# Kernel optimization log

Hardware: AMD Instinct MI355X
Metric: run time of the kernel (lower is better)

Reference implementation:

```python
import jax, jax.numpy as jnp
import numpy as np

L, H, D, E, V, MAXS = 12, 12, 64, 768, 50257, 1024

def _ln(x, g, b, eps=1e-5):
    m = jnp.mean(x, axis=-1, keepdims=True)
    v = jnp.mean(jnp.square(x - m), axis=-1, keepdims=True)
    return (x - m) * jax.lax.rsqrt(v + eps) * g + b

def setup_inputs() -> dict:
    key = jax.random.key(0)
    ks = jax.random.split(key, 16)
    s = 0.02
    inp = {
        "input_ids": jax.random.randint(ks[0], (1, 1), 0, V),
        "past_key": jax.random.normal(ks[1], (L, 1, H, MAXS, D), jnp.float32),
        "past_value": jax.random.normal(ks[2], (L, 1, H, MAXS, D), jnp.float32),
        "past_seq_len": 1023,
        "attention_mask": jnp.ones((1, MAXS), jnp.float32),
        "wte": jax.random.normal(ks[3], (V, E), jnp.float32) * s,
        "wpe": jax.random.normal(ks[4], (MAXS, E), jnp.float32) * s,
        "ln1_g": jnp.ones((L, E), jnp.float32),
        "ln1_b": jnp.zeros((L, E), jnp.float32),
        "attn_w": jax.random.normal(ks[5], (L, E, 3 * E), jnp.float32) * s,
        "attn_b": jnp.zeros((L, 3 * E), jnp.float32),
        "proj_w": jax.random.normal(ks[6], (L, E, E), jnp.float32) * s,
        "proj_b": jnp.zeros((L, E), jnp.float32),
        "ln2_g": jnp.ones((L, E), jnp.float32),
        "ln2_b": jnp.zeros((L, E), jnp.float32),
        "fc_w": jax.random.normal(ks[7], (L, E, 4 * E), jnp.float32) * s,
        "fc_b": jnp.zeros((L, 4 * E), jnp.float32),
        "mlp_w": jax.random.normal(ks[8], (L, 4 * E, E), jnp.float32) * s,
        "mlp_b": jnp.zeros((L, E), jnp.float32),
        "lnf_g": jnp.ones((E,), jnp.float32),
        "lnf_b": jnp.zeros((E,), jnp.float32),
    }
    return inp

def reference(input_ids, past_key, past_value, past_seq_len, attention_mask,
              wte, wpe, ln1_g, ln1_b, attn_w, attn_b, proj_w, proj_b,
              ln2_g, ln2_b, fc_w, fc_b, mlp_w, mlp_b, lnf_g, lnf_b):
    S = int(past_seq_len)  # static cache length
    h = wte[input_ids] + wpe[S]                      # [1,1,E]
    bias = (1.0 - attention_mask[:, :S + 1]) * -1e9  # [1,S+1]
    scale = 1.0 / jnp.sqrt(jnp.float32(D))
    pk, pv = past_key, past_value
    for l in range(L):
        x = _ln(h, ln1_g[l], ln1_b[l])
        qkv = x @ attn_w[l] + attn_b[l]              # [1,1,3E]
        q, k, v = jnp.split(qkv, 3, axis=-1)
        q = q.reshape(1, 1, H, D).transpose(0, 2, 1, 3)  # [1,H,1,D]
        k = k.reshape(1, 1, H, D).transpose(0, 2, 1, 3)
        v = v.reshape(1, 1, H, D).transpose(0, 2, 1, 3)
        k_full = jnp.concatenate([pk[l, :, :, :S, :], k], axis=2)  # [1,H,S+1,D]
        v_full = jnp.concatenate([pv[l, :, :, :S, :], v], axis=2)
        scores = jnp.einsum('bhqd,bhkd->bhqk', q, k_full) * scale
        scores = scores + bias[:, None, None, :]
        attn = jax.nn.softmax(scores, axis=-1)
        o = jnp.einsum('bhqk,bhkd->bhqd', attn, v_full)
        o = o.transpose(0, 2, 1, 3).reshape(1, 1, H * D)
        h = h + o @ proj_w[l] + proj_b[l]
        x2 = _ln(h, ln2_g[l], ln2_b[l])
        h = h + jax.nn.gelu(x2 @ fc_w[l] + fc_b[l], approximate=True) @ mlp_w[l] + mlp_b[l]
        pk = pk.at[l, :, :, S, :].set(k[:, :, 0, :])
        pv = pv.at[l, :, :, S, :].set(v[:, :, 0, :])
    h = _ln(h, lnf_g, lnf_b)
    logits = h @ wte.T                               # [1,1,V] (tied lm_head)
    return (logits, pk, pv)
```

## Files before the change

kernel.cpp:

```cpp
#include <hip/hip_runtime.h>
#include <math.h>

#define EMB 768
#define NH 12
#define HD 64
#define NL 12
#define NV 50257
#define MAXS 1024
#define S_PAST 1023
#define E3 2304
#define E4 3072

#define WS_H    0
#define WS_QKV  768
#define WS_FC   3072
#define WS_PART 6144

__device__ __forceinline__ void blockReduce2(float& a, float& b, volatile float* ra, volatile float* rb) {
  int lane = threadIdx.x & 63, wid = threadIdx.x >> 6;
#pragma unroll
  for (int o = 32; o > 0; o >>= 1) { a += __shfl_down(a, o); b += __shfl_down(b, o); }
  if (lane == 0) { ra[wid] = a; rb[wid] = b; }
  __syncthreads();
  if (threadIdx.x == 0) {
    ra[0] = ra[0] + ra[1] + ra[2] + ra[3];
    rb[0] = rb[0] + rb[1] + rb[2] + rb[3];
  }
  __syncthreads();
  a = ra[0]; b = rb[0];
}

__global__ void init_kernel(const int* __restrict__ ids, const float* __restrict__ wte,
                            const float* __restrict__ wpe, const float* __restrict__ attn_b,
                            float* __restrict__ hvec, float* __restrict__ qkv) {
  int idx = blockIdx.x * 256 + threadIdx.x;
  if (idx < E3) qkv[idx] = attn_b[idx];
  if (idx < EMB) {
    int id = ids[0];
    hvec[idx] = wte[(size_t)id * EMB + idx] + wpe[(size_t)S_PAST * EMB + idx];
  }
}

__global__ void ln_gemv4(const float* __restrict__ hvec, const float* __restrict__ g,
                         const float* __restrict__ bb, const float* __restrict__ W,
                         float* __restrict__ out, int N, int l) {
  __shared__ float lh[EMB];
  __shared__ float xs[32];
  __shared__ float ra[4], rb[4];
  __shared__ float4 red[4][64];
  int tid = threadIdx.x, lane = tid & 63, wid = tid >> 6;
  int e0 = blockIdx.y * 32;
  float hv0 = hvec[tid], hv1 = hvec[tid + 256], hv2 = hvec[tid + 512];
  int j4 = blockIdx.x * 64 + lane;
  int N4 = N >> 2;
  const float4* p = (const float4*)(W + (size_t)l * EMB * N) + (size_t)(e0 + wid) * N4 + j4;
  float4 w[8];
#pragma unroll
  for (int i = 0; i < 8; i++) w[i] = p[(size_t)(i * 4) * N4];
  float gv = 0.f, bv = 0.f;
  if (tid < 32) { gv = g[l * EMB + e0 + tid]; bv = bb[l * EMB + e0 + tid]; }
  lh[tid] = hv0; lh[tid + 256] = hv1; lh[tid + 512] = hv2;
  float s1 = hv0 + hv1 + hv2;
  float s2 = hv0 * hv0 + hv1 * hv1 + hv2 * hv2;
  blockReduce2(s1, s2, ra, rb);
  float mean = s1 * (1.f / EMB);
  float var = s2 * (1.f / EMB) - mean * mean;
  float rstd = rsqrtf(var + 1e-5f);
  if (tid < 32) xs[tid] = (lh[e0 + tid] - mean) * rstd * gv + bv;
  __syncthreads();
  float4 acc = {0.f, 0.f, 0.f, 0.f};
#pragma unroll
  for (int i = 0; i < 8; i++) {
    float x = xs[wid + i * 4];
    acc.x += x * w[i].x; acc.y += x * w[i].y; acc.z += x * w[i].z; acc.w += x * w[i].w;
  }
  red[wid][lane] = acc;
  __syncthreads();
  if (wid == 0) {
    float4 a0 = red[0][lane], a1 = red[1][lane], a2 = red[2][lane], a3 = red[3][lane];
    float rx = a0.x + a1.x + a2.x + a3.x;
    float ry = a0.y + a1.y + a2.y + a3.y;
    float rz = a0.z + a1.z + a2.z + a3.z;
    float rw = a0.w + a1.w + a2.w + a3.w;
    float* op = out + (size_t)j4 * 4;
    atomicAdd(op + 0, rx); atomicAdd(op + 1, ry);
    atomicAdd(op + 2, rz); atomicAdd(op + 3, rw);
  }
}

__global__ void attn_kv(const float* __restrict__ qkv, const float* __restrict__ pk,
                        const float* __restrict__ pv, const float* __restrict__ mask,
                        float* __restrict__ opk, float* __restrict__ opv,
                        float* __restrict__ part, int l) {
  int h = blockIdx.x >> 4, c = blockIdx.x & 15;
  int tid = threadIdx.x, lane = tid & 63, wid = tid >> 6;
  int sub = tid & 15, grp = tid >> 4;
  __shared__ float4 qs4[16];
  __shared__ float sc[64];
  __shared__ float4 redo[4][16];
  if (tid < 16) qs4[tid] = ((const float4*)(qkv + h * 64))[tid];
  __syncthreads();
  size_t base = ((size_t)(l * NH + h) * MAXS) * HD;
  const float4* K4 = (const float4*)(pk + base);
  const float4* V4 = (const float4*)(pv + base);
  float4* oK4 = (float4*)(opk + base);
  float4* oV4 = (float4*)(opv + base);
  int t0 = c * 64;
  float4 kreg[4];
#pragma unroll
  for (int i = 0; i < 4; i++) {
    int t = t0 + grp + i * 16;
    kreg[i] = (t == S_PAST) ? ((const float4*)(qkv + EMB + h * 64))[sub] : K4[(size_t)t * 16 + sub];
  }
#pragma unroll
  for (int i = 0; i < 4; i++) {
    int t = t0 + grp + i * 16;
    oK4[(size_t)t * 16 + sub] = kreg[i];
  }
  float4 q4 = qs4[sub];
#pragma unroll
  for (int i = 0; i < 4; i++) {
    int key = grp + i * 16;
    float p = q4.x * kreg[i].x + q4.y * kreg[i].y + q4.z * kreg[i].z + q4.w * kreg[i].w;
    p += __shfl_xor(p, 1); p += __shfl_xor(p, 2);
    p += __shfl_xor(p, 4); p += __shfl_xor(p, 8);
    if (sub == 0) sc[key] = p * 0.125f + (1.f - mask[t0 + key]) * (-1e9f);
  }
  __syncthreads();
  if (wid == 0) {
    float a = sc[lane];
    float m = a;
#pragma unroll
    for (int o = 32; o > 0; o >>= 1) m = fmaxf(m, __shfl_down(m, o));
    m = __shfl(m, 0);
    float ea = expf(a - m);
    sc[lane] = ea;
    float s = ea;
#pragma unroll
    for (int o = 32; o > 0; o >>= 1) s += __shfl_down(s, o);
    if (lane == 0) { part[(h * 16 + c) * 68 + 0] = m; part[(h * 16 + c) * 68 + 1] = s; }
  }
  __syncthreads();
  float4 vreg[4];
#pragma unroll
  for (int i = 0; i < 4; i++) {
    int t = t0 + grp + i * 16;
    vreg[i] = (t == S_PAST) ? ((const float4*)(qkv + 2 * EMB + h * 64))[sub] : V4[(size_t)t * 16 + sub];
  }
#pragma unroll
  for (int i = 0; i < 4; i++) {
    int t = t0 + grp + i * 16;
    oV4[(size_t)t * 16 + sub] = vreg[i];
  }
  float4 acc = {0.f, 0.f, 0.f, 0.f};
#pragma unroll
  for (int i = 0; i < 4; i++) {
    float w = sc[grp + i * 16];
    acc.x += w * vreg[i].x; acc.y += w * vreg[i].y; acc.z += w * vreg[i].z; acc.w += w * vreg[i].w;
  }
  acc.x += __shfl_xor(acc.x, 16); acc.y += __shfl_xor(acc.y, 16);
  acc.z += __shfl_xor(acc.z, 16); acc.w += __shfl_xor(acc.w, 16);
  acc.x += __shfl_xor(acc.x, 32); acc.y += __shfl_xor(acc.y, 32);
  acc.z += __shfl_xor(acc.z, 32); acc.w += __shfl_xor(acc.w, 32);
  if (lane < 16) redo[wid][lane] = acc;
  __syncthreads();
  if (tid < 16) {
    float4 a0 = redo[0][tid], a1 = redo[1][tid], a2 = redo[2][tid], a3 = redo[3][tid];
    float4 r;
    r.x = a0.x + a1.x + a2.x + a3.x;
    r.y = a0.y + a1.y + a2.y + a3.y;
    r.z = a0.z + a1.z + a2.z + a3.z;
    r.w = a0.w + a1.w + a2.w + a3.w;
    ((float4*)(part + (h * 16 + c) * 68 + 4))[tid] = r;
  }
}

__global__ void proj_attn(const float* __restrict__ part, const float* __restrict__ W,
                          const float* __restrict__ bias, const float* __restrict__ fc_b,
                          float* __restrict__ hout, float* __restrict__ wfc, int l) {
  int jb = blockIdx.x;
  int rt = blockIdx.y;
  int h = rt >> 2, esub = rt & 3;
  int tid = threadIdx.x, lane = tid & 63, wid = tid >> 6;
  __shared__ float xs[16];
  __shared__ float4 red[4][64];
  int j4 = jb * 64 + lane;
  const int N4 = EMB >> 2;
  int r0 = h * 64 + esub * 16;
  const float4* p = (const float4*)(W + (size_t)l * EMB * EMB) + (size_t)(r0 + wid) * N4 + j4;
  float4 w[4];
#pragma unroll
  for (int i = 0; i < 4; i++) w[i] = p[(size_t)(i * 4) * N4];
  if (tid < 16) {
    float M = -1e30f;
#pragma unroll
    for (int q = 0; q < 16; q++) M = fmaxf(M, part[(h * 16 + q) * 68]);
    float T = 0.f, o = 0.f;
    int d = esub * 16 + tid;
#pragma unroll
    for (int q = 0; q < 16; q++) {
      float wq = expf(part[(h * 16 + q) * 68] - M);
      T += part[(h * 16 + q) * 68 + 1] * wq;
      o += part[(h * 16 + q) * 68 + 4 + d] * wq;
    }
    xs[tid] = o / T;
  }
  int bid = rt * 3 + jb;
  if (bid < 12) wfc[bid * 256 + tid] = fc_b[l * E4 + bid * 256 + tid];
  __syncthreads();
  float4 acc = {0.f, 0.f, 0.f, 0.f};
#pragma unroll
  for (int i = 0; i < 4; i++) {
    float x = xs[wid + i * 4];
    acc.x += x * w[i].x; acc.y += x * w[i].y; acc.z += x * w[i].z; acc.w += x * w[i].w;
  }
  red[wid][lane] = acc;
  __syncthreads();
  if (wid == 0) {
    float4 a0 = red[0][lane], a1 = red[1][lane], a2 = red[2][lane], a3 = red[3][lane];
    float rx = a0.x + a1.x + a2.x + a3.x;
    float ry = a0.y + a1.y + a2.y + a3.y;
    float rz = a0.z + a1.z + a2.z + a3.z;
    float rw = a0.w + a1.w + a2.w + a3.w;
    if (rt == 0) {
      const float* bp = bias + l * EMB + jb * 256 + lane * 4;
      rx += bp[0]; ry += bp[1]; rz += bp[2]; rw += bp[3];
    }
    float* op = hout + (size_t)jb * 256 + (size_t)lane * 4;
    atomicAdd(op + 0, rx); atomicAdd(op + 1, ry);
    atomicAdd(op + 2, rz); atomicAdd(op + 3, rw);
  }
}

__global__ void mlp_gemv4(const float* __restrict__ fcv, const float* __restrict__ W,
                          const float* __restrict__ bias, const float* __restrict__ attn_b,
                          float* __restrict__ hout, float* __restrict__ qkv, int l) {
  __shared__ float xs[64];
  __shared__ float4 red[4][64];
  int tid = threadIdx.x, lane = tid & 63, wid = tid >> 6;
  int e0 = blockIdx.y * 64;
  int j4 = blockIdx.x * 64 + lane;
  const int N4 = EMB >> 2;
  const float4* p = (const float4*)(W + (size_t)l * E4 * EMB) + (size_t)(e0 + wid) * N4 + j4;
  float4 w[16];
#pragma unroll
  for (int i = 0; i < 16; i++) w[i] = p[(size_t)(i * 4) * N4];
  if (tid < 64) {
    float x = fcv[e0 + tid];
    xs[tid] = 0.5f * x * (1.f + tanhf(0.7978845608028654f * (x + 0.044715f * x * x * x)));
  }
  int bid = blockIdx.y * 3 + blockIdx.x;
  if (l + 1 < NL && bid < 9) qkv[bid * 256 + tid] = attn_b[(l + 1) * E3 + bid * 256 + tid];
  __syncthreads();
  float4 acc = {0.f, 0.f, 0.f, 0.f};
#pragma unroll
  for (int i = 0; i < 16; i++) {
    float x = xs[wid + i * 4];
    acc.x += x * w[i].x; acc.y += x * w[i].y; acc.z += x * w[i].z; acc.w += x * w[i].w;
  }
  red[wid][lane] = acc;
  __syncthreads();
  if (wid == 0) {
    float4 a0 = red[0][lane], a1 = red[1][lane], a2 = red[2][lane], a3 = red[3][lane];
    float rx = a0.x + a1.x + a2.x + a3.x;
    float ry = a0.y + a1.y + a2.y + a3.y;
    float rz = a0.z + a1.z + a2.z + a3.z;
    float rw = a0.w + a1.w + a2.w + a3.w;
    if (blockIdx.y == 0) {
      const float* bp = bias + l * EMB + j4 * 4;
      rx += bp[0]; ry += bp[1]; rz += bp[2]; rw += bp[3];
    }
    float* op = hout + (size_t)j4 * 4;
    atomicAdd(op + 0, rx); atomicAdd(op + 1, ry);
    atomicAdd(op + 2, rz); atomicAdd(op + 3, rw);
  }
}

__global__ void logits_lnf(const float* __restrict__ hvec, const float* __restrict__ g,
                           const float* __restrict__ b, const float* __restrict__ wte,
                           float* __restrict__ out) {
  __shared__ float4 xs4[192];
  __shared__ float ra[4], rb[4];
  int tid = threadIdx.x, lane = tid & 63, wid = tid >> 6;
  float hv0 = hvec[tid], hv1 = hvec[tid + 256], hv2 = hvec[tid + 512];
  int v = blockIdx.x * 4 + wid;
  float4 a0 = {0,0,0,0}, a1 = {0,0,0,0}, a2 = {0,0,0,0};
  if (v < NV) {
    const float4* row = (const float4*)(wte + (size_t)v * EMB);
    a0 = row[lane]; a1 = row[lane + 64]; a2 = row[lane + 128];
  }
  float s1 = hv0 + hv1 + hv2;
  float s2 = hv0 * hv0 + hv1 * hv1 + hv2 * hv2;
  blockReduce2(s1, s2, ra, rb);
  float mean = s1 * (1.f / EMB);
  float var = s2 * (1.f / EMB) - mean * mean;
  float rstd = rsqrtf(var + 1e-5f);
  ((float*)xs4)[tid]       = (hv0 - mean) * rstd * g[tid]       + b[tid];
  ((float*)xs4)[tid + 256] = (hv1 - mean) * rstd * g[tid + 256] + b[tid + 256];
  ((float*)xs4)[tid + 512] = (hv2 - mean) * rstd * g[tid + 512] + b[tid + 512];
  __syncthreads();
  if (v >= NV) return;
  float4 x0 = xs4[lane], x1 = xs4[lane + 64], x2 = xs4[lane + 128];
  float acc = a0.x * x0.x + a0.y * x0.y + a0.z * x0.z + a0.w * x0.w
            + a1.x * x1.x + a1.y * x1.y + a1.z * x1.z + a1.w * x1.w
            + a2.x * x2.x + a2.y * x2.y + a2.z * x2.z + a2.w * x2.w;
#pragma unroll
  for (int o = 32; o > 0; o >>= 1) acc += __shfl_down(acc, o);
  if (lane == 0) out[v] = acc;
}

extern "C" void kernel_launch(void* const* d_in, const int* in_sizes, int n_in,
                              void* d_out, int out_size, void* d_ws, size_t ws_size,
                              hipStream_t stream) {
  const int* input_ids = (const int*)d_in[0];
  const float* past_key = (const float*)d_in[1];
  const float* past_value = (const float*)d_in[2];
  const float* mask = (const float*)d_in[4];
  const float* wte = (const float*)d_in[5];
  const float* wpe = (const float*)d_in[6];
  const float* ln1_g = (const float*)d_in[7];
  const float* ln1_b = (const float*)d_in[8];
  const float* attn_w = (const float*)d_in[9];
  const float* attn_b = (const float*)d_in[10];
  const float* proj_w = (const float*)d_in[11];
  const float* proj_b = (const float*)d_in[12];
  const float* ln2_g = (const float*)d_in[13];
  const float* ln2_b = (const float*)d_in[14];
  const float* fc_w = (const float*)d_in[15];
  const float* fc_b = (const float*)d_in[16];
  const float* mlp_w = (const float*)d_in[17];
  const float* mlp_b = (const float*)d_in[18];
  const float* lnf_g = (const float*)d_in[19];
  const float* lnf_b = (const float*)d_in[20];

  float* out = (float*)d_out;
  float* out_logits = out;
  float* out_pk = out + NV;
  float* out_pv = out_pk + (size_t)NL * NH * MAXS * HD;

  float* ws = (float*)d_ws;
  float* wh = ws + WS_H;
  float* wqkv = ws + WS_QKV;
  float* wfc = ws + WS_FC;
  float* wpart = ws + WS_PART;

  init_kernel<<<9, 256, 0, stream>>>(input_ids, wte, wpe, attn_b, wh, wqkv);

  for (int l = 0; l < NL; l++) {
    ln_gemv4<<<dim3(9, 24), 256, 0, stream>>>(wh, ln1_g, ln1_b, attn_w, wqkv, E3, l);
    attn_kv<<<192, 256, 0, stream>>>(wqkv, past_key, past_value, mask, out_pk, out_pv, wpart, l);
    proj_attn<<<dim3(3, 48), 256, 0, stream>>>(wpart, proj_w, proj_b, fc_b, wh, wfc, l);
    ln_gemv4<<<dim3(12, 24), 256, 0, stream>>>(wh, ln2_g, ln2_b, fc_w, wfc, E4, l);
    mlp_gemv4<<<dim3(3, 48), 256, 0, stream>>>(wfc, mlp_w, mlp_b, attn_b, wh, wqkv, l);
  }
  logits_lnf<<<12565, 256, 0, stream>>>(wh, lnf_g, lnf_b, wte, out_logits);
}
```

Measured before the change: 448.5 us.

## Fuse per-layer kernels into two launches with per-head dataflow counters

Merges the five per-layer kernels into two. Kernel A runs the QKV producer, the attention chunks and the output projection, and kernel B runs FC and MLP. Dependent blocks spin on global atomic counters per head or tile instead of waiting at kernel boundaries. The K/V cache copy loads are issued before the wait, so they overlap with producer work. This cuts launch overhead and inter-kernel bubbles, but risks deadlock or stalls if waiting blocks take up CUs before their producers are scheduled.

```diff
diff --git a/kernel.cpp b/kernel.cpp
--- a/kernel.cpp
+++ b/kernel.cpp
@@ -11,10 +11,32 @@
 #define E3 2304
 #define E4 3072
 
+typedef unsigned int u32;
+
 #define WS_H    0
 #define WS_QKV  768
 #define WS_FC   3072
 #define WS_PART 6144
+#define WS_CNT  19200
+#define CNT_WORDS 6912
+
+__device__ __forceinline__ void f4add(float4& a, const float4& b) {
+  a.x += b.x; a.y += b.y; a.z += b.z; a.w += b.w;
+}
+
+__device__ __forceinline__ void bump(u32* cnt) {
+  __threadfence();
+  __syncthreads();
+  if (threadIdx.x == 0)
+    __hip_atomic_fetch_add(cnt, 1u, __ATOMIC_RELEASE, __HIP_MEMORY_SCOPE_AGENT);
+}
+__device__ __forceinline__ void wait_cnt(u32* cnt, u32 n) {
+  if (threadIdx.x == 0) {
+    while (__hip_atomic_load(cnt, __ATOMIC_ACQUIRE, __HIP_MEMORY_SCOPE_AGENT) < n)
+      __builtin_amdgcn_s_sleep(2);
+  }
+  __syncthreads();
+}
 
 __device__ __forceinline__ void blockReduce2(float& a, float& b, volatile float* ra, volatile float* rb) {
   int lane = threadIdx.x & 63, wid = threadIdx.x >> 6;
@@ -30,110 +52,140 @@
   a = ra[0]; b = rb[0];
 }
 
+__device__ __forceinline__ float gelu(float x) {
+  return 0.5f * x * (1.f + tanhf(0.7978845608028654f * (x + 0.044715f * x * x * x)));
+}
+
 __global__ void init_kernel(const int* __restrict__ ids, const float* __restrict__ wte,
-                            const float* __restrict__ wpe, const float* __restrict__ attn_b,
-                            float* __restrict__ hvec, float* __restrict__ qkv) {
-  int idx = blockIdx.x * 256 + threadIdx.x;
-  if (idx < E3) qkv[idx] = attn_b[idx];
-  if (idx < EMB) {
+                            const float* __restrict__ wpe, float* __restrict__ wsf) {
+  int tid = threadIdx.x;
+  if (blockIdx.x < 3) {
+    int e = blockIdx.x * 256 + tid;
     int id = ids[0];
-    hvec[idx] = wte[(size_t)id * EMB + idx] + wpe[(size_t)S_PAST * EMB + idx];
-  }
-}
-
-__global__ void ln_gemv4(const float* __restrict__ hvec, const float* __restrict__ g,
-                         const float* __restrict__ bb, const float* __restrict__ W,
-                         float* __restrict__ out, int N, int l) {
-  __shared__ float lh[EMB];
-  __shared__ float xs[32];
-  __shared__ float ra[4], rb[4];
-  __shared__ float4 red[4][64];
-  int tid = threadIdx.x, lane = tid & 63, wid = tid >> 6;
-  int e0 = blockIdx.y * 32;
+    wsf[WS_H + e] = wte[(size_t)id * EMB + e] + wpe[(size_t)S_PAST * EMB + e];
+  } else {
+    u32* c = (u32*)(wsf + WS_CNT);
+    for (int k = tid; k < CNT_WORDS; k += 256) c[k] = 0;
+  }
+}
+
+
+__device__ void phase_producer(int p, const float* __restrict__ hvec,
+                               const float* __restrict__ g, const float* __restrict__ bb,
+                               const float* __restrict__ W, const float* __restrict__ qb,
+                               float* __restrict__ wsqkv, float* __restrict__ opk,
+                               float* __restrict__ opv, int l, float* smem, u32* prodc) {
+  int h = p / 6, r = p % 6;
+  int cq = (r >> 1) * EMB + h * 64 + (r & 1) * 32;
+  int tid = threadIdx.x;
+  float* lh = smem;
+  float* xs = smem + 768;
+  volatile float* ra = smem + 1536; volatile float* rb = smem + 1540;
+  float4* red = (float4*)(smem + 1544);
+  int col4 = tid & 7, grp = tid >> 3;
   float hv0 = hvec[tid], hv1 = hvec[tid + 256], hv2 = hvec[tid + 512];
-  int j4 = blockIdx.x * 64 + lane;
-  int N4 = N >> 2;
-  const float4* p = (const float4*)(W + (size_t)l * EMB * N) + (size_t)(e0 + wid) * N4 + j4;
-  float4 w[8];
-#pragma unroll
-  for (int i = 0; i < 8; i++) w[i] = p[(size_t)(i * 4) * N4];
-  float gv = 0.f, bv = 0.f;
-  if (tid < 32) { gv = g[l * EMB + e0 + tid]; bv = bb[l * EMB + e0 + tid]; }
+  const float4* W4 = (const float4*)(W + (size_t)l * EMB * E3) + (cq >> 2) + col4;
+  float4 w[12];
+#pragma unroll
+  for (int i = 0; i < 12; i++) w[i] = W4[(size_t)(grp + 32 * i) * (E3 >> 2)];
+  float gv0 = g[l * EMB + tid], gv1 = g[l * EMB + tid + 256], gv2 = g[l * EMB + tid + 512];
+  float bv0 = bb[l * EMB + tid], bv1 = bb[l * EMB + tid + 256], bv2 = bb[l * EMB + tid + 512];
   lh[tid] = hv0; lh[tid + 256] = hv1; lh[tid + 512] = hv2;
-  float s1 = hv0 + hv1 + hv2;
-  float s2 = hv0 * hv0 + hv1 * hv1 + hv2 * hv2;
+  float s1 = hv0 + hv1 + hv2, s2 = hv0 * hv0 + hv1 * hv1 + hv2 * hv2;
   blockReduce2(s1, s2, ra, rb);
   float mean = s1 * (1.f / EMB);
   float var = s2 * (1.f / EMB) - mean * mean;
   float rstd = rsqrtf(var + 1e-5f);
-  if (tid < 32) xs[tid] = (lh[e0 + tid] - mean) * rstd * gv + bv;
+  xs[tid]       = (hv0 - mean) * rstd * gv0 + bv0;
+  xs[tid + 256] = (hv1 - mean) * rstd * gv1 + bv1;
+  xs[tid + 512] = (hv2 - mean) * rstd * gv2 + bv2;
   __syncthreads();
   float4 acc = {0.f, 0.f, 0.f, 0.f};
 #pragma unroll
-  for (int i = 0; i < 8; i++) {
-    float x = xs[wid + i * 4];
+  for (int i = 0; i < 12; i++) {
+    float x = xs[grp + 32 * i];
     acc.x += x * w[i].x; acc.y += x * w[i].y; acc.z += x * w[i].z; acc.w += x * w[i].w;
   }
-  red[wid][lane] = acc;
-  __syncthreads();
-  if (wid == 0) {
-    float4 a0 = red[0][lane], a1 = red[1][lane], a2 = red[2][lane], a3 = red[3][lane];
-    float rx = a0.x + a1.x + a2.x + a3.x;
-    float ry = a0.y + a1.y + a2.y + a3.y;
-    float rz = a0.z + a1.z + a2.z + a3.z;
-    float rw = a0.w + a1.w + a2.w + a3.w;
-    float* op = out + (size_t)j4 * 4;
-    atomicAdd(op + 0, rx); atomicAdd(op + 1, ry);
-    atomicAdd(op + 2, rz); atomicAdd(op + 3, rw);
-  }
-}
-
-__global__ void attn_kv(const float* __restrict__ qkv, const float* __restrict__ pk,
-                        const float* __restrict__ pv, const float* __restrict__ mask,
-                        float* __restrict__ opk, float* __restrict__ opv,
-                        float* __restrict__ part, int l) {
-  int h = blockIdx.x >> 4, c = blockIdx.x & 15;
+#pragma unroll
+  for (int i = 0; i < 12; i++) w[i] = W4[(size_t)(grp + 32 * (i + 12)) * (E3 >> 2)];
+#pragma unroll
+  for (int i = 0; i < 12; i++) {
+    float x = xs[grp + 32 * (i + 12)];
+    acc.x += x * w[i].x; acc.y += x * w[i].y; acc.z += x * w[i].z; acc.w += x * w[i].w;
+  }
+  red[tid] = acc;
+  __syncthreads();
+#pragma unroll
+  for (int s = 128; s >= 8; s >>= 1) {
+    if (tid < s) f4add(red[tid], red[tid + s]);
+    __syncthreads();
+  }
+  if (tid < 8) {
+    float4 o = red[tid];
+    f4add(o, ((const float4*)(qb + l * E3 + cq))[tid]);
+    ((float4*)wsqkv)[(cq >> 2) + tid] = o;
+    if (r >= 2) {
+      size_t base = ((size_t)(l * NH + h) * MAXS) * HD;
+      float* dst = (r < 4) ? opk : opv;
+      ((float4*)(dst + base))[(size_t)S_PAST * 16 + (r & 1) * 8 + tid] = o;
+    }
+  }
+  bump(prodc);
+}
+
+__device__ void phase_attn(int a, const float* __restrict__ wsqkv,
+                           const float* __restrict__ pk, const float* __restrict__ pv,
+                           const float* __restrict__ mask, float* __restrict__ opk,
+                           float* __restrict__ opv, float* __restrict__ part,
+                           int l, float* smem, u32* prodc, u32* chc) {
+  int h = a >> 4, c = a & 15;
   int tid = threadIdx.x, lane = tid & 63, wid = tid >> 6;
   int sub = tid & 15, grp = tid >> 4;
-  __shared__ float4 qs4[16];
-  __shared__ float sc[64];
-  __shared__ float4 redo[4][16];
-  if (tid < 16) qs4[tid] = ((const float4*)(qkv + h * 64))[tid];
-  __syncthreads();
+  float4* qs4 = (float4*)smem;
+  float* sc = smem + 64;
+  float4* redo = (float4*)(smem + 128);
   size_t base = ((size_t)(l * NH + h) * MAXS) * HD;
   const float4* K4 = (const float4*)(pk + base);
   const float4* V4 = (const float4*)(pv + base);
-  float4* oK4 = (float4*)(opk + base);
-  float4* oV4 = (float4*)(opv + base);
   int t0 = c * 64;
-  float4 kreg[4];
+  float4 kreg[4], vreg[4];
 #pragma unroll
   for (int i = 0; i < 4; i++) {
     int t = t0 + grp + i * 16;
-    kreg[i] = (t == S_PAST) ? ((const float4*)(qkv + EMB + h * 64))[sub] : K4[(size_t)t * 16 + sub];
+    if (t != S_PAST) { kreg[i] = K4[(size_t)t * 16 + sub]; vreg[i] = V4[(size_t)t * 16 + sub]; }
+  }
+  wait_cnt(prodc, 6);
+  if (tid < 16) qs4[tid] = ((const float4*)(wsqkv + h * 64))[tid];
+  __syncthreads();
+  if (c == 15 && grp == 15) {
+    kreg[3] = ((const float4*)(wsqkv + EMB + h * 64))[sub];
+    vreg[3] = ((const float4*)(wsqkv + 2 * EMB + h * 64))[sub];
   }
 #pragma unroll
   for (int i = 0; i < 4; i++) {
     int t = t0 + grp + i * 16;
-    oK4[(size_t)t * 16 + sub] = kreg[i];
+    if (t != S_PAST) {
+      ((float4*)(opk + base))[(size_t)t * 16 + sub] = kreg[i];
+      ((float4*)(opv + base))[(size_t)t * 16 + sub] = vreg[i];
+    }
   }
   float4 q4 = qs4[sub];
 #pragma unroll
   for (int i = 0; i < 4; i++) {
     int key = grp + i * 16;
-    float p = q4.x * kreg[i].x + q4.y * kreg[i].y + q4.z * kreg[i].z + q4.w * kreg[i].w;
-    p += __shfl_xor(p, 1); p += __shfl_xor(p, 2);
-    p += __shfl_xor(p, 4); p += __shfl_xor(p, 8);
-    if (sub == 0) sc[key] = p * 0.125f + (1.f - mask[t0 + key]) * (-1e9f);
+    float pp = q4.x * kreg[i].x + q4.y * kreg[i].y + q4.z * kreg[i].z + q4.w * kreg[i].w;
+    pp += __shfl_xor(pp, 1); pp += __shfl_xor(pp, 2);
+    pp += __shfl_xor(pp, 4); pp += __shfl_xor(pp, 8);
+    if (sub == 0) sc[key] = pp * 0.125f + (1.f - mask[t0 + key]) * (-1e9f);
   }
   __syncthreads();
   if (wid == 0) {
-    float a = sc[lane];
-    float m = a;
+    float aa = sc[lane];
+    float m = aa;
 #pragma unroll
     for (int o = 32; o > 0; o >>= 1) m = fmaxf(m, __shfl_down(m, o));
     m = __shfl(m, 0);
-    float ea = expf(a - m);
+    float ea = expf(aa - m);
     sc[lane] = ea;
     float s = ea;
 #pragma unroll
@@ -141,17 +193,6 @@
     if (lane == 0) { part[(h * 16 + c) * 68 + 0] = m; part[(h * 16 + c) * 68 + 1] = s; }
   }
   __syncthreads();
-  float4 vreg[4];
-#pragma unroll
-  for (int i = 0; i < 4; i++) {
-    int t = t0 + grp + i * 16;
-    vreg[i] = (t == S_PAST) ? ((const float4*)(qkv + 2 * EMB + h * 64))[sub] : V4[(size_t)t * 16 + sub];
-  }
-#pragma unroll
-  for (int i = 0; i < 4; i++) {
-    int t = t0 + grp + i * 16;
-    oV4[(size_t)t * 16 + sub] = vreg[i];
-  }
   float4 acc = {0.f, 0.f, 0.f, 0.f};
 #pragma unroll
   for (int i = 0; i < 4; i++) {
@@ -162,28 +203,29 @@
   acc.z += __shfl_xor(acc.z, 16); acc.w += __shfl_xor(acc.w, 16);
   acc.x += __shfl_xor(acc.x, 32); acc.y += __shfl_xor(acc.y, 32);
   acc.z += __shfl_xor(acc.z, 32); acc.w += __shfl_xor(acc.w, 32);
-  if (lane < 16) redo[wid][lane] = acc;
+  if (lane < 16) redo[wid * 16 + lane] = acc;
   __syncthreads();
   if (tid < 16) {
-    float4 a0 = redo[0][tid], a1 = redo[1][tid], a2 = redo[2][tid], a3 = redo[3][tid];
-    float4 r;
-    r.x = a0.x + a1.x + a2.x + a3.x;
-    r.y = a0.y + a1.y + a2.y + a3.y;
-    r.z = a0.z + a1.z + a2.z + a3.z;
-    r.w = a0.w + a1.w + a2.w + a3.w;
-    ((float4*)(part + (h * 16 + c) * 68 + 4))[tid] = r;
-  }
-}
-
-__global__ void proj_attn(const float* __restrict__ part, const float* __restrict__ W,
-                          const float* __restrict__ bias, const float* __restrict__ fc_b,
-                          float* __restrict__ hout, float* __restrict__ wfc, int l) {
-  int jb = blockIdx.x;
-  int rt = blockIdx.y;
+    float4 a0 = redo[tid], a1 = redo[16 + tid], a2 = redo[32 + tid], a3 = redo[48 + tid];
+    float4 rr;
+    rr.x = a0.x + a1.x + a2.x + a3.x;
+    rr.y = a0.y + a1.y + a2.y + a3.y;
+    rr.z = a0.z + a1.z + a2.z + a3.z;
+    rr.w = a0.w + a1.w + a2.w + a3.w;
+    ((float4*)(part + (h * 16 + c) * 68 + 4))[tid] = rr;
+  }
+  bump(chc);
+}
+
+__device__ void phase_proj(int pi, const float* __restrict__ part, const float* __restrict__ W,
+                           const float* __restrict__ bias, const float* __restrict__ fc_b,
+                           float* __restrict__ hout, float* __restrict__ wfc,
+                           int l, float* smem, u32* chc) {
+  int jb = pi % 3, rt = pi / 3;
   int h = rt >> 2, esub = rt & 3;
   int tid = threadIdx.x, lane = tid & 63, wid = tid >> 6;
-  __shared__ float xs[16];
-  __shared__ float4 red[4][64];
+  float* xs = smem;
+  float4* red = (float4*)(smem + 16);
   int j4 = jb * 64 + lane;
   const int N4 = EMB >> 2;
   int r0 = h * 64 + esub * 16;
@@ -191,6 +233,8 @@
   float4 w[4];
 #pragma unroll
   for (int i = 0; i < 4; i++) w[i] = p[(size_t)(i * 4) * N4];
+  if (pi < 12) wfc[pi * 256 + tid] = fc_b[l * E4 + pi * 256 + tid];
+  wait_cnt(chc, 16);
   if (tid < 16) {
     float M = -1e30f;
 #pragma unroll
@@ -205,8 +249,6 @@
     }
     xs[tid] = o / T;
   }
-  int bid = rt * 3 + jb;
-  if (bid < 12) wfc[bid * 256 + tid] = fc_b[l * E4 + bid * 256 + tid];
   __syncthreads();
   float4 acc = {0.f, 0.f, 0.f, 0.f};
 #pragma unroll
@@ -214,10 +256,10 @@
     float x = xs[wid + i * 4];
     acc.x += x * w[i].x; acc.y += x * w[i].y; acc.z += x * w[i].z; acc.w += x * w[i].w;
   }
-  red[wid][lane] = acc;
+  red[wid * 64 + lane] = acc;
   __syncthreads();
   if (wid == 0) {
-    float4 a0 = red[0][lane], a1 = red[1][lane], a2 = red[2][lane], a3 = red[3][lane];
+    float4 a0 = red[lane], a1 = red[64 + lane], a2 = red[128 + lane], a3 = red[192 + lane];
     float rx = a0.x + a1.x + a2.x + a3.x;
     float ry = a0.y + a1.y + a2.y + a3.y;
     float rz = a0.z + a1.z + a2.z + a3.z;
@@ -232,54 +274,137 @@
   }
 }
 
-__global__ void mlp_gemv4(const float* __restrict__ fcv, const float* __restrict__ W,
-                          const float* __restrict__ bias, const float* __restrict__ attn_b,
-                          float* __restrict__ hout, float* __restrict__ qkv, int l) {
-  __shared__ float xs[64];
-  __shared__ float4 red[4][64];
-  int tid = threadIdx.x, lane = tid & 63, wid = tid >> 6;
-  int e0 = blockIdx.y * 64;
-  int j4 = blockIdx.x * 64 + lane;
-  const int N4 = EMB >> 2;
-  const float4* p = (const float4*)(W + (size_t)l * E4 * EMB) + (size_t)(e0 + wid) * N4 + j4;
-  float4 w[16];
-#pragma unroll
-  for (int i = 0; i < 16; i++) w[i] = p[(size_t)(i * 4) * N4];
-  if (tid < 64) {
-    float x = fcv[e0 + tid];
-    xs[tid] = 0.5f * x * (1.f + tanhf(0.7978845608028654f * (x + 0.044715f * x * x * x)));
-  }
-  int bid = blockIdx.y * 3 + blockIdx.x;
-  if (l + 1 < NL && bid < 9) qkv[bid * 256 + tid] = attn_b[(l + 1) * E3 + bid * 256 + tid];
-  __syncthreads();
-  float4 acc = {0.f, 0.f, 0.f, 0.f};
-#pragma unroll
-  for (int i = 0; i < 16; i++) {
-    float x = xs[wid + i * 4];
-    acc.x += x * w[i].x; acc.y += x * w[i].y; acc.z += x * w[i].z; acc.w += x * w[i].w;
-  }
-  red[wid][lane] = acc;
-  __syncthreads();
-  if (wid == 0) {
-    float4 a0 = red[0][lane], a1 = red[1][lane], a2 = red[2][lane], a3 = red[3][lane];
-    float rx = a0.x + a1.x + a2.x + a3.x;
-    float ry = a0.y + a1.y + a2.y + a3.y;
-    float rz = a0.z + a1.z + a2.z + a3.z;
-    float rw = a0.w + a1.w + a2.w + a3.w;
-    if (blockIdx.y == 0) {
-      const float* bp = bias + l * EMB + j4 * 4;
-      rx += bp[0]; ry += bp[1]; rz += bp[2]; rw += bp[3];
-    }
-    float* op = hout + (size_t)j4 * 4;
-    atomicAdd(op + 0, rx); atomicAdd(op + 1, ry);
-    atomicAdd(op + 2, rz); atomicAdd(op + 3, rw);
+__global__ __launch_bounds__(256, 2) void kA(
+    const float* __restrict__ pk, const float* __restrict__ pv, const float* __restrict__ mask,
+    const float* __restrict__ ln1_g, const float* __restrict__ ln1_b,
+    const float* __restrict__ attn_w, const float* __restrict__ attn_b,
+    const float* __restrict__ proj_w, const float* __restrict__ proj_b,
+    const float* __restrict__ fc_b, float* __restrict__ opk, float* __restrict__ opv,
+    float* __restrict__ wsf, int l) {
+  __shared__ __align__(16) float smem[2568];
+  u32* cnt = (u32*)(wsf + WS_CNT);
+  u32* prodc = cnt;
+  u32* chc = cnt + 2304;
+  float* wh = wsf + WS_H;
+  float* wqkv = wsf + WS_QKV;
+  float* wfc = wsf + WS_FC;
+  float* wpart = wsf + WS_PART;
+  int bi = blockIdx.x;
+  if (bi < 72) {
+    int h = bi / 6;
+    phase_producer(bi, wh, ln1_g, ln1_b, attn_w, attn_b, wqkv, opk, opv, l, smem,
+                   prodc + (l * 12 + h) * 16);
+  } else if (bi < 264) {
+    int a = bi - 72;
+    int h = a >> 4;
+    phase_attn(a, wqkv, pk, pv, mask, opk, opv, wpart, l, smem,
+               prodc + (l * 12 + h) * 16, chc + (l * 12 + h) * 16);
+  } else {
+    int pi = bi - 264;
+    int h = (pi / 3) >> 2;
+    phase_proj(pi, wpart, proj_w, proj_b, fc_b, wh, wfc, l, smem,
+               chc + (l * 12 + h) * 16);
+  }
+}
+
+
+__global__ __launch_bounds__(256, 2) void kB(
+    const float* __restrict__ ln2_g, const float* __restrict__ ln2_b,
+    const float* __restrict__ fc_w, const float* __restrict__ mlp_w,
+    const float* __restrict__ mlp_b, float* __restrict__ wsf, int l) {
+  __shared__ __align__(16) float smem[1840];
+  u32* fcc = (u32*)(wsf + WS_CNT) + 4608;
+  float* wh = wsf + WS_H;
+  float* wfc = wsf + WS_FC;
+  int bi = blockIdx.x, tid = threadIdx.x, lane = tid & 63, wid = tid >> 6;
+  if (bi < 288) {
+    int jt = bi % 12, et = bi / 12;
+    float* lh = smem;
+    float* xs = smem + 768;
+    volatile float* ra = smem + 800; volatile float* rb = smem + 804;
+    float4* red = (float4*)(smem + 816);
+    int e0 = et * 32;
+    float hv0 = wh[tid], hv1 = wh[tid + 256], hv2 = wh[tid + 512];
+    int j4 = jt * 64 + lane;
+    const int N4 = E4 >> 2;
+    const float4* p = (const float4*)(fc_w + (size_t)l * EMB * E4) + (size_t)(e0 + wid) * N4 + j4;
+    float4 w[8];
+#pragma unroll
+    for (int i = 0; i < 8; i++) w[i] = p[(size_t)(i * 4) * N4];
+    float gv = 0.f, bv = 0.f;
+    if (tid < 32) { gv = ln2_g[l * EMB + e0 + tid]; bv = ln2_b[l * EMB + e0 + tid]; }
+    lh[tid] = hv0; lh[tid + 256] = hv1; lh[tid + 512] = hv2;
+    float s1 = hv0 + hv1 + hv2, s2 = hv0 * hv0 + hv1 * hv1 + hv2 * hv2;
+    blockReduce2(s1, s2, ra, rb);
+    float mean = s1 * (1.f / EMB);
+    float var = s2 * (1.f / EMB) - mean * mean;
+    float rstd = rsqrtf(var + 1e-5f);
+    if (tid < 32) xs[tid] = (lh[e0 + tid] - mean) * rstd * gv + bv;
+    __syncthreads();
+    float4 acc = {0.f, 0.f, 0.f, 0.f};
+#pragma unroll
+    for (int i = 0; i < 8; i++) {
+      float x = xs[wid + i * 4];
+      acc.x += x * w[i].x; acc.y += x * w[i].y; acc.z += x * w[i].z; acc.w += x * w[i].w;
+    }
+    red[wid * 64 + lane] = acc;
+    __syncthreads();
+    if (wid == 0) {
+      float4 a0 = red[lane], a1 = red[64 + lane], a2 = red[128 + lane], a3 = red[192 + lane];
+      float rx = a0.x + a1.x + a2.x + a3.x;
+      float ry = a0.y + a1.y + a2.y + a3.y;
+      float rz = a0.z + a1.z + a2.z + a3.z;
+      float rw = a0.w + a1.w + a2.w + a3.w;
+      float* op = wfc + (size_t)j4 * 4;
+      atomicAdd(op + 0, rx); atomicAdd(op + 1, ry);
+      atomicAdd(op + 2, rz); atomicAdd(op + 3, rw);
+    }
+    bump(fcc + (l * 12 + jt) * 16);
+  } else {
+    int m = bi - 288;
+    int jt3 = m % 3, et2 = m / 3;
+    int jtf = et2 >> 2;
+    float* xs = smem;
+    float4* red = (float4*)(smem + 64);
+    int e0 = et2 * 64;
+    int j4 = jt3 * 64 + lane;
+    const int N4 = EMB >> 2;
+    const float4* p = (const float4*)(mlp_w + (size_t)l * E4 * EMB) + (size_t)(e0 + wid) * N4 + j4;
+    float4 w[16];
+#pragma unroll
+    for (int i = 0; i < 16; i++) w[i] = p[(size_t)(i * 4) * N4];
+    wait_cnt(fcc + (l * 12 + jtf) * 16, 24);
+    if (tid < 64) xs[tid] = gelu(wfc[e0 + tid]);
+    __syncthreads();
+    float4 acc = {0.f, 0.f, 0.f, 0.f};
+#pragma unroll
+    for (int i = 0; i < 16; i++) {
+      float x = xs[wid + i * 4];
+      acc.x += x * w[i].x; acc.y += x * w[i].y; acc.z += x * w[i].z; acc.w += x * w[i].w;
+    }
+    red[wid * 64 + lane] = acc;
+    __syncthreads();
+    if (wid == 0) {
+      float4 a0 = red[lane], a1 = red[64 + lane], a2 = red[128 + lane], a3 = red[192 + lane];
+      float rx = a0.x + a1.x + a2.x + a3.x;
+      float ry = a0.y + a1.y + a2.y + a3.y;
+      float rz = a0.z + a1.z + a2.z + a3.z;
+      float rw = a0.w + a1.w + a2.w + a3.w;
+      if (et2 == 0) {
+        const float* bp = mlp_b + l * EMB + j4 * 4;
+        rx += bp[0]; ry += bp[1]; rz += bp[2]; rw += bp[3];
+      }
+      float* op = wsf + WS_H + (size_t)j4 * 4;
+      atomicAdd(op + 0, rx); atomicAdd(op + 1, ry);
+      atomicAdd(op + 2, rz); atomicAdd(op + 3, rw);
+    }
   }
 }
 
 __global__ void logits_lnf(const float* __restrict__ hvec, const float* __restrict__ g,
                            const float* __restrict__ b, const float* __restrict__ wte,
                            float* __restrict__ out) {
-  __shared__ float4 xs4[192];
+  __shared__ __align__(16) float4 xs4[192];
   __shared__ float ra[4], rb[4];
   int tid = threadIdx.x, lane = tid & 63, wid = tid >> 6;
   float hv0 = hvec[tid], hv1 = hvec[tid + 256], hv2 = hvec[tid + 512];
@@ -337,21 +462,14 @@
   float* out_logits = out;
   float* out_pk = out + NV;
   float* out_pv = out_pk + (size_t)NL * NH * MAXS * HD;
-
-  float* ws = (float*)d_ws;
-  float* wh = ws + WS_H;
-  float* wqkv = ws + WS_QKV;
-  float* wfc = ws + WS_FC;
-  float* wpart = ws + WS_PART;
-
-  init_kernel<<<9, 256, 0, stream>>>(input_ids, wte, wpe, attn_b, wh, wqkv);
+  float* wsf = (float*)d_ws;
+
+  init_kernel<<<4, 256, 0, stream>>>(input_ids, wte, wpe, wsf);
 
   for (int l = 0; l < NL; l++) {
-    ln_gemv4<<<dim3(9, 24), 256, 0, stream>>>(wh, ln1_g, ln1_b, attn_w, wqkv, E3, l);
-    attn_kv<<<192, 256, 0, stream>>>(wqkv, past_key, past_value, mask, out_pk, out_pv, wpart, l);
-    proj_attn<<<dim3(3, 48), 256, 0, stream>>>(wpart, proj_w, proj_b, fc_b, wh, wfc, l);
-    ln_gemv4<<<dim3(12, 24), 256, 0, stream>>>(wh, ln2_g, ln2_b, fc_w, wfc, E4, l);
-    mlp_gemv4<<<dim3(3, 48), 256, 0, stream>>>(wfc, mlp_w, mlp_b, attn_b, wh, wqkv, l);
-  }
-  logits_lnf<<<12565, 256, 0, stream>>>(wh, lnf_g, lnf_b, wte, out_logits);
-}
+    kA<<<408, 256, 0, stream>>>(past_key, past_value, mask, ln1_g, ln1_b, attn_w, attn_b,
+                                proj_w, proj_b, fc_b, out_pk, out_pv, wsf, l);
+    kB<<<432, 256, 0, stream>>>(ln2_g, ln2_b, fc_w, mlp_w, mlp_b, wsf, l);
+  }
+  logits_lnf<<<12565, 256, 0, stream>>>(wsf + WS_H, lnf_g, lnf_b, wte, out_logits);
+}
```

Measured after the change: 1.598 ms. 3.56x slower.
